# Optimization experiments

Hardware: AMD Instinct MI355X
Metric: run time of the kernel (lower is better)

Reference implementation:

```python
import jax, jax.numpy as jnp
import numpy as np

B, T, C, H = 4, 2048, 1024, 16
D = C // H  # head_dim = 64

def setup_inputs() -> dict:
    key = jax.random.key(0)
    k1, k2, k3 = jax.random.split(key, 3)
    x = jax.random.normal(k1, (B, T, C), dtype=jnp.float32)
    w_qkv = jax.random.normal(k2, (C, 3 * C), dtype=jnp.float32) * (C ** -0.5)
    w_proj = jax.random.normal(k3, (C, C), dtype=jnp.float32) * (C ** -0.5)
    b_proj = jnp.zeros((C,), dtype=jnp.float32)
    return {"x": x, "w_qkv": w_qkv, "w_proj": w_proj, "b_proj": b_proj}

def reference(x, w_qkv, w_proj, b_proj):
    Bx, Tx, Cx = x.shape
    qkv = x @ w_qkv  # [B,T,3C]
    q, k, v = jnp.split(qkv, 3, axis=-1)
    # [B,T,H,D] -> [B,H,T,D]
    q = q.reshape(Bx, Tx, H, D).transpose(0, 2, 1, 3)
    k = k.reshape(Bx, Tx, H, D).transpose(0, 2, 1, 3)
    v = v.reshape(Bx, Tx, H, D).transpose(0, 2, 1, 3)
    scale = 1.0 / np.sqrt(D).astype(np.float32)
    att = jnp.einsum('bhqd,bhkd->bhqk', q, k) * scale  # [B,H,T,T]
    causal = jnp.tril(jnp.ones((Tx, Tx), dtype=bool))
    att = jnp.where(causal, att, -jnp.inf)
    att = jax.nn.softmax(att, axis=-1)
    y = jnp.einsum('bhqk,bhkd->bhqd', att, v)  # [B,H,T,D]
    y = y.transpose(0, 2, 1, 3).reshape(Bx, Tx, Cx)
    return y @ w_proj + b_proj
```

## Files before the change

### kernel.cpp

```cpp
#include <hip/hip_runtime.h>

typedef unsigned short u16;
typedef unsigned int u32;
typedef __attribute__((ext_vector_type(2))) unsigned int u32x2;
typedef __attribute__((ext_vector_type(8))) short bf16x8;
typedef __attribute__((ext_vector_type(4))) float f32x4;
typedef __attribute__((ext_vector_type(16))) float f32x16;
typedef __attribute__((ext_vector_type(4))) unsigned short u16x4;

#define MFMA16(a, b, c) __builtin_amdgcn_mfma_f32_16x16x32_bf16((a), (b), (c), 0, 0, 0)
#define MFMA32(a, b, c) __builtin_amdgcn_mfma_f32_32x32x16_bf16((a), (b), (c), 0, 0, 0)

__device__ __forceinline__ u16 f2bf(float f) {
  union { float f; unsigned int i; } v; v.f = f;
  return (u16)((v.i + 0x7FFFu + ((v.i >> 16) & 1u)) >> 16);
}
__device__ __forceinline__ float exp2a(float x) {
  float r; asm("v_exp_f32 %0, %1" : "=v"(r) : "v"(x)); return r;
}
__device__ __forceinline__ u32 cvtpk(float lo, float hi) {
  u32 d; asm("v_cvt_pk_bf16_f32 %0, %1, %2" : "=v"(d) : "v"(lo), "v"(hi)); return d;
}
__device__ __forceinline__ void gl2lds16(const u16* g, u16* l) {
  __builtin_amdgcn_global_load_lds(
      (const __attribute__((address_space(1))) void*)g,
      (__attribute__((address_space(3))) void*)l, 16, 0, 0);
}

__global__ __launch_bounds__(256) void k_prep(const float* __restrict__ x,
                                              u16* __restrict__ xb,
                                              const float* __restrict__ w_qkv,
                                              u16* __restrict__ wqkvT,
                                              const float* __restrict__ w_proj,
                                              u16* __restrict__ wprojT) {
  const int id = (int)blockIdx.x;
  const int t = threadIdx.x;
  if (id < 4096) {
    const int i = id * 256 + t;
    const float* s = x + (size_t)i * 8;
    float4 a = *(const float4*)(s);
    float4 b = *(const float4*)(s + 4);
    union { u16 o[8]; int4 v; } u;
    u.o[0] = f2bf(a.x); u.o[1] = f2bf(a.y); u.o[2] = f2bf(a.z); u.o[3] = f2bf(a.w);
    u.o[4] = f2bf(b.x); u.o[5] = f2bf(b.y); u.o[6] = f2bf(b.z); u.o[7] = f2bf(b.w);
    *(int4*)(&xb[(size_t)i * 8]) = u.v;
    return;
  }
  __shared__ u16 tile[64][65];
  const float* src;
  u16* dst;
  int R, C, c0, r0;
  if (id < 4864) {
    const int q = id - 4096;
    src = w_qkv; dst = wqkvT; R = 1024; C = 3072;
    c0 = (q % 48) * 64; r0 = (q / 48) * 64;
  } else {
    const int q = id - 4864;
    src = w_proj; dst = wprojT; R = 1024; C = 1024;
    c0 = (q % 16) * 64; r0 = (q / 16) * 64;
  }
#pragma unroll
  for (int i = 0; i < 16; ++i) {
    int e = i * 256 + t, rr = e >> 6, cc = e & 63;
    tile[rr][cc] = f2bf(src[(size_t)(r0 + rr) * C + c0 + cc]);
  }
  __syncthreads();
#pragma unroll
  for (int i = 0; i < 16; ++i) {
    int e = i * 256 + t, rr = e >> 6, cc = e & 63;
    dst[(size_t)(c0 + rr) * R + r0 + cc] = tile[cc][rr];
  }
}

template <int QKV>
__global__ __launch_bounds__(256) void k_gemm(
    const u16* __restrict__ A, const u16* __restrict__ Bt,
    const float* __restrict__ bias, float* __restrict__ Cf,
    u16* __restrict__ Qb, u16* __restrict__ Kb, u16* __restrict__ VTb,
    int M, int N, int K, int BNn) {
  __shared__ __attribute__((aligned(16))) u16 As[128 * 32];
  __shared__ __attribute__((aligned(16))) u16 Bs[128 * 32];
  const int wg = (int)blockIdx.x;
  const int xcd = wg & 7, loc = wg >> 3;
  const int bmPerXcd = (M >> 7) >> 3;
  const int bm = xcd * bmPerXcd + loc / BNn;
  const int bn = loc % BNn;
  const int t = threadIdx.x, lane = t & 63, w = t >> 6;
  const int wr = w >> 1, wc = w & 1;
  const int rh = lane & 15, kg = lane >> 4;
  const int srow = lane >> 2, sk8 = (lane & 3) << 3;

  f32x4 acc[4][4];
#pragma unroll
  for (int mi = 0; mi < 4; ++mi)
#pragma unroll
    for (int ni = 0; ni < 4; ++ni) acc[mi][ni] = (f32x4)0.0f;

  for (int k0 = 0; k0 < K; k0 += 32) {
#pragma unroll
    for (int i = 0; i < 2; ++i) {
      const int r0 = w * 32 + i * 16;
      gl2lds16(&A[(size_t)(bm * 128 + r0 + srow) * K + k0 + sk8], &As[r0 * 32]);
      gl2lds16(&Bt[(size_t)(bn * 128 + r0 + srow) * K + k0 + sk8], &Bs[r0 * 32]);
    }
    asm volatile("s_waitcnt vmcnt(0)" ::: "memory");
    __syncthreads();

    bf16x8 af[4], bfr[4];
#pragma unroll
    for (int mi = 0; mi < 4; ++mi)
      af[mi] = *(const bf16x8*)(&As[(wr * 64 + mi * 16 + rh) * 32 + kg * 8]);
#pragma unroll
    for (int ni = 0; ni < 4; ++ni)
      bfr[ni] = *(const bf16x8*)(&Bs[(wc * 64 + ni * 16 + rh) * 32 + kg * 8]);
    __builtin_amdgcn_s_setprio(1);
#pragma unroll
    for (int mi = 0; mi < 4; ++mi)
#pragma unroll
      for (int ni = 0; ni < 4; ++ni)
        acc[mi][ni] = MFMA16(af[mi], bfr[ni], acc[mi][ni]);
    __builtin_amdgcn_s_setprio(0);
    __syncthreads();
  }

  if (QKV == 0) {
    const int rbase = bm * 128 + wr * 64;
    const int cbase = bn * 128 + wc * 64;
#pragma unroll
    for (int ni = 0; ni < 4; ++ni) {
      const int col = cbase + ni * 16 + rh;
      const float bv = bias ? bias[col] : 0.0f;
#pragma unroll
      for (int mi = 0; mi < 4; ++mi) {
#pragma unroll
        for (int r = 0; r < 4; ++r) {
          int row = rbase + mi * 16 + kg * 4 + r;
          Cf[(size_t)row * N + col] = acc[mi][ni][r] + bv;
        }
      }
    }
  } else {
    const float SCQ = 0.125f * 1.44269504f;
    const int rowbase = bm * 128 + wr * 64;
    const int b = rowbase >> 11;
    const int tb = rowbase & 2047;
    const int cbase = bn * 128 + wc * 64;
    const int role = cbase >> 10;
    const int h = (cbase & 1023) >> 6;
    const int bh = b * 16 + h;
#pragma unroll
    for (int ni = 0; ni < 4; ++ni) {
      const int d = ni * 16 + rh;
#pragma unroll
      for (int mi = 0; mi < 4; ++mi) {
        const int tt = tb + mi * 16 + kg * 4;
        if (role == 2) {
          u16x4 pk;
#pragma unroll
          for (int r = 0; r < 4; ++r) pk[r] = f2bf(acc[mi][ni][r]);
          *(u16x4*)(&VTb[((size_t)bh * 64 + d) * 2048 + tt]) = pk;
        } else {
          u16* dst = (role == 0) ? Qb : Kb;
          const float sc = (role == 0) ? SCQ : 1.0f;
#pragma unroll
          for (int r = 0; r < 4; ++r)
            dst[((size_t)bh * 2048 + tt + r) * 64 + d] = f2bf(acc[mi][ni][r] * sc);
        }
      }
    }
  }
}

__global__ __launch_bounds__(64, 2) void k_attn(const u16* __restrict__ Qb,
                                                const u16* __restrict__ Kb,
                                                const u16* __restrict__ VTb,
                                                u16* __restrict__ Y) {
  const int bh = blockIdx.x;
  const int sb = 31 - (int)blockIdx.y;
  const int lane = threadIdx.x & 63;
  const int q31 = lane & 31, hi = lane >> 5;
  const int qA = sb * 64 + q31;
  const int qBr = sb * 64 + 32 + q31;
  const u16* Qh = Qb + (size_t)bh * 2048 * 64;
  const u16* Kh = Kb + (size_t)bh * 2048 * 64;
  const u16* Vh = VTb + (size_t)bh * 64 * 2048;
  const int b = bh >> 4, h = bh & 15;

  bf16x8 qfA[4], qfB[4];
#pragma unroll
  for (int d = 0; d < 4; ++d) {
    qfA[d] = *(const bf16x8*)(&Qh[(size_t)qA * 64 + d * 16 + hi * 8]);
    qfB[d] = *(const bf16x8*)(&Qh[(size_t)qBr * 64 + d * 16 + hi * 8]);
  }

  f32x16 oA0 = (f32x16)0.0f, oA1 = (f32x16)0.0f;
  f32x16 oB0 = (f32x16)0.0f, oB1 = (f32x16)0.0f;
  float mA = -1e30f, sA = 0.0f, mB = -1e30f, sB = 0.0f;

  const int nt = 2 * sb + 2;
  bf16x8 kf[4];
#pragma unroll
  for (int d = 0; d < 4; ++d)
    kf[d] = *(const bf16x8*)(&Kh[(size_t)q31 * 64 + d * 16 + hi * 8]);

  for (int tt = 0; tt < nt; ++tt) {
    const int j0 = tt * 32;
    const bool aAct = tt < nt - 1;

    const int jn = (tt + 1 < nt) ? j0 + 32 : j0;
    bf16x8 kn[4];
#pragma unroll
    for (int d = 0; d < 4; ++d)
      kn[d] = *(const bf16x8*)(&Kh[(size_t)(jn + q31) * 64 + d * 16 + hi * 8]);
    const bf16x8 vf0 = *(const bf16x8*)(&Vh[(size_t)q31 * 2048 + j0 + hi * 8]);
    const bf16x8 vf1 = *(const bf16x8*)(&Vh[(size_t)q31 * 2048 + j0 + 16 + hi * 8]);
    const bf16x8 vf2 = *(const bf16x8*)(&Vh[(size_t)(32 + q31) * 2048 + j0 + hi * 8]);
    const bf16x8 vf3 = *(const bf16x8*)(&Vh[(size_t)(32 + q31) * 2048 + j0 + 16 + hi * 8]);

    f32x16 stB = (f32x16)0.0f;
    __builtin_amdgcn_s_setprio(1);
#pragma unroll
    for (int d = 0; d < 4; ++d) stB = MFMA32(kf[d], qfB[d], stB);
    f32x16 stA = (f32x16)0.0f;
    if (aAct) {
#pragma unroll
      for (int d = 0; d < 4; ++d) stA = MFMA32(kf[d], qfA[d], stA);
    }
    __builtin_amdgcn_s_setprio(0);

    if (tt == nt - 2) {
#pragma unroll
      for (int r = 0; r < 16; ++r) {
        const int kcol = (r & 3) + 8 * (r >> 2) + 4 * hi;
        if (kcol > q31) stA[r] = -1e30f;
      }
    }
    if (tt == nt - 1) {
#pragma unroll
      for (int r = 0; r < 16; ++r) {
        const int kcol = (r & 3) + 8 * (r >> 2) + 4 * hi;
        if (kcol > q31) stB[r] = -1e30f;
      }
    }

    union { u32 w4[4]; bf16x8 f; } paA0, paA1, paB0, paB1;
    if (aAct) {
      float mx = fmaxf(
          fmaxf(fmaxf(fmaxf(stA[0], stA[1]), fmaxf(stA[2], stA[3])),
                fmaxf(fmaxf(stA[4], stA[5]), fmaxf(stA[6], stA[7]))),
          fmaxf(fmaxf(fmaxf(stA[8], stA[9]), fmaxf(stA[10], stA[11])),
                fmaxf(fmaxf(stA[12], stA[13]), fmaxf(stA[14], stA[15]))));
      if (__any(mx - mA > 8.0f)) {
        mx = fmaxf(mx, __shfl_xor(mx, 32));
        const float mn = fmaxf(mA, mx);
        const float scf = exp2a(mA - mn);
        mA = mn; sA *= scf; oA0 *= scf; oA1 *= scf;
      }
      float p[16];
#pragma unroll
      for (int r = 0; r < 16; ++r) p[r] = exp2a(stA[r] - mA);
      sA += (((p[0] + p[1]) + (p[2] + p[3])) + ((p[4] + p[5]) + (p[6] + p[7]))) +
            (((p[8] + p[9]) + (p[10] + p[11])) + ((p[12] + p[13]) + (p[14] + p[15])));
      u32 D0 = cvtpk(p[0], p[1]),   D1 = cvtpk(p[2], p[3]);
      u32 D2 = cvtpk(p[4], p[5]),   D3 = cvtpk(p[6], p[7]);
      u32 D4 = cvtpk(p[8], p[9]),   D5 = cvtpk(p[10], p[11]);
      u32 D6 = cvtpk(p[12], p[13]), D7 = cvtpk(p[14], p[15]);
      u32x2 s02 = __builtin_amdgcn_permlane32_swap(D0, D2, false, false);
      u32x2 s13 = __builtin_amdgcn_permlane32_swap(D1, D3, false, false);
      u32x2 s46 = __builtin_amdgcn_permlane32_swap(D4, D6, false, false);
      u32x2 s57 = __builtin_amdgcn_permlane32_swap(D5, D7, false, false);
      paA0.w4[0] = s02.x; paA0.w4[1] = s13.x; paA0.w4[2] = s02.y; paA0.w4[3] = s13.y;
      paA1.w4[0] = s46.x; paA1.w4[1] = s57.x; paA1.w4[2] = s46.y; paA1.w4[3] = s57.y;
    }

    {
      float mx = fmaxf(
          fmaxf(fmaxf(fmaxf(stB[0], stB[1]), fmaxf(stB[2], stB[3])),
                fmaxf(fmaxf(stB[4], stB[5]), fmaxf(stB[6], stB[7]))),
          fmaxf(fmaxf(fmaxf(stB[8], stB[9]), fmaxf(stB[10], stB[11])),
                fmaxf(fmaxf(stB[12], stB[13]), fmaxf(stB[14], stB[15]))));
      if (__any(mx - mB > 8.0f)) {
        mx = fmaxf(mx, __shfl_xor(mx, 32));
        const float mn = fmaxf(mB, mx);
        const float scf = exp2a(mB - mn);
        mB = mn; sB *= scf; oB0 *= scf; oB1 *= scf;
      }
      float p[16];
#pragma unroll
      for (int r = 0; r < 16; ++r) p[r] = exp2a(stB[r] - mB);
      sB += (((p[0] + p[1]) + (p[2] + p[3])) + ((p[4] + p[5]) + (p[6] + p[7]))) +
            (((p[8] + p[9]) + (p[10] + p[11])) + ((p[12] + p[13]) + (p[14] + p[15])));
      u32 D0 = cvtpk(p[0], p[1]),   D1 = cvtpk(p[2], p[3]);
      u32 D2 = cvtpk(p[4], p[5]),   D3 = cvtpk(p[6], p[7]);
      u32 D4 = cvtpk(p[8], p[9]),   D5 = cvtpk(p[10], p[11]);
      u32 D6 = cvtpk(p[12], p[13]), D7 = cvtpk(p[14], p[15]);
      u32x2 s02 = __builtin_amdgcn_permlane32_swap(D0, D2, false, false);
      u32x2 s13 = __builtin_amdgcn_permlane32_swap(D1, D3, false, false);
      u32x2 s46 = __builtin_amdgcn_permlane32_swap(D4, D6, false, false);
      u32x2 s57 = __builtin_amdgcn_permlane32_swap(D5, D7, false, false);
      paB0.w4[0] = s02.x; paB0.w4[1] = s13.x; paB0.w4[2] = s02.y; paB0.w4[3] = s13.y;
      paB1.w4[0] = s46.x; paB1.w4[1] = s57.x; paB1.w4[2] = s46.y; paB1.w4[3] = s57.y;
    }

    __builtin_amdgcn_s_setprio(1);
    oB0 = MFMA32(vf0, paB0.f, oB0);
    oB0 = MFMA32(vf1, paB1.f, oB0);
    oB1 = MFMA32(vf2, paB0.f, oB1);
    oB1 = MFMA32(vf3, paB1.f, oB1);
    if (aAct) {
      oA0 = MFMA32(vf0, paA0.f, oA0);
      oA0 = MFMA32(vf1, paA1.f, oA0);
      oA1 = MFMA32(vf2, paA0.f, oA1);
      oA1 = MFMA32(vf3, paA1.f, oA1);
    }
    __builtin_amdgcn_s_setprio(0);

#pragma unroll
    for (int d = 0; d < 4; ++d) kf[d] = kn[d];
  }

  sA += __shfl_xor(sA, 32);
  sB += __shfl_xor(sB, 32);
  const float invA = 1.0f / sA, invB = 1.0f / sB;
  u16* yrowA = Y + ((size_t)b * 2048 + qA) * 1024 + h * 64;
  u16* yrowB = Y + ((size_t)b * 2048 + qBr) * 1024 + h * 64;
#pragma unroll
  for (int a = 0; a < 4; ++a) {
    u16x4 pk;
#pragma unroll
    for (int i = 0; i < 4; ++i) pk[i] = f2bf(oA0[a * 4 + i] * invA);
    *(u16x4*)(yrowA + a * 8 + 4 * hi) = pk;
#pragma unroll
    for (int i = 0; i < 4; ++i) pk[i] = f2bf(oA1[a * 4 + i] * invA);
    *(u16x4*)(yrowA + 32 + a * 8 + 4 * hi) = pk;
#pragma unroll
    for (int i = 0; i < 4; ++i) pk[i] = f2bf(oB0[a * 4 + i] * invB);
    *(u16x4*)(yrowB + a * 8 + 4 * hi) = pk;
#pragma unroll
    for (int i = 0; i < 4; ++i) pk[i] = f2bf(oB1[a * 4 + i] * invB);
    *(u16x4*)(yrowB + 32 + a * 8 + 4 * hi) = pk;
  }
}

extern "C" void kernel_launch(void* const* d_in, const int* in_sizes, int n_in,
                              void* d_out, int out_size, void* d_ws, size_t ws_size,
                              hipStream_t stream) {
  const float* x      = (const float*)d_in[0];
  const float* w_qkv  = (const float*)d_in[1];
  const float* w_proj = (const float*)d_in[2];
  const float* b_proj = (const float*)d_in[3];
  float* out = (float*)d_out;

  char* ws = (char*)d_ws;
  u16* wqkvT  = (u16*)(ws);
  u16* wprojT = (u16*)(ws + 6291456);
  u16* Qb     = (u16*)(ws + 8388608);
  u16* Kb     = (u16*)(ws + 25165824);
  u16* VTb    = (u16*)(ws + 41943040);
  u16* xb     = (u16*)(ws + 58720256);
  u16* Yb     = xb;

  k_prep<<<5120, 256, 0, stream>>>(x, xb, w_qkv, wqkvT, w_proj, wprojT);
  k_gemm<1><<<1536, 256, 0, stream>>>(xb, wqkvT, nullptr, nullptr,
                                      Qb, Kb, VTb, 8192, 3072, 1024, 24);
  k_attn<<<dim3(64, 32), 64, 0, stream>>>(Qb, Kb, VTb, Yb);
  k_gemm<0><<<512, 256, 0, stream>>>(Yb, wprojT, b_proj, out,
                                     nullptr, nullptr, nullptr, 8192, 1024, 1024, 8);
}
```

Measured before the change: 200.9 us.

## Software-pipeline attention loop so PV MFMAs of previous tile overlap current QK

Restructures the causal flash-attention inner loop into a prologue, steady state and epilogue. In the steady state the P·V MFMAs for the previous key tile are issued right after the Q·K MFMAs for the current tile. The softmax exp and convert work of one tile can then overlap matrix-core work of another, instead of serialising on the dependency chain. This costs extra live registers for the carried P fragments and duplicated code, which may raise VGPR pressure and reduce occupancy.

```diff
diff --git a/kernel.cpp b/kernel.cpp
--- a/kernel.cpp
+++ b/kernel.cpp
@@ -198,53 +198,36 @@
   float mA = -1e30f, sA = 0.0f, mB = -1e30f, sB = 0.0f;
 
   const int nt = 2 * sb + 2;
-  bf16x8 kf[4];
+  bf16x8 kf[4], kn[4];
 #pragma unroll
   for (int d = 0; d < 4; ++d)
     kf[d] = *(const bf16x8*)(&Kh[(size_t)q31 * 64 + d * 16 + hi * 8]);
 
-  for (int tt = 0; tt < nt; ++tt) {
-    const int j0 = tt * 32;
-    const bool aAct = tt < nt - 1;
-
-    const int jn = (tt + 1 < nt) ? j0 + 32 : j0;
-    bf16x8 kn[4];
+  union U { u32 w4[4]; bf16x8 f; };
+  U paA0, paA1, paB0, paB1;
+
+  {
 #pragma unroll
     for (int d = 0; d < 4; ++d)
-      kn[d] = *(const bf16x8*)(&Kh[(size_t)(jn + q31) * 64 + d * 16 + hi * 8]);
-    const bf16x8 vf0 = *(const bf16x8*)(&Vh[(size_t)q31 * 2048 + j0 + hi * 8]);
-    const bf16x8 vf1 = *(const bf16x8*)(&Vh[(size_t)q31 * 2048 + j0 + 16 + hi * 8]);
-    const bf16x8 vf2 = *(const bf16x8*)(&Vh[(size_t)(32 + q31) * 2048 + j0 + hi * 8]);
-    const bf16x8 vf3 = *(const bf16x8*)(&Vh[(size_t)(32 + q31) * 2048 + j0 + 16 + hi * 8]);
+      kn[d] = *(const bf16x8*)(&Kh[(size_t)(32 + q31) * 64 + d * 16 + hi * 8]);
 
     f32x16 stB = (f32x16)0.0f;
     __builtin_amdgcn_s_setprio(1);
 #pragma unroll
     for (int d = 0; d < 4; ++d) stB = MFMA32(kf[d], qfB[d], stB);
     f32x16 stA = (f32x16)0.0f;
-    if (aAct) {
-#pragma unroll
-      for (int d = 0; d < 4; ++d) stA = MFMA32(kf[d], qfA[d], stA);
-    }
+#pragma unroll
+    for (int d = 0; d < 4; ++d) stA = MFMA32(kf[d], qfA[d], stA);
     __builtin_amdgcn_s_setprio(0);
 
-    if (tt == nt - 2) {
+    if (nt == 2) {
 #pragma unroll
       for (int r = 0; r < 16; ++r) {
         const int kcol = (r & 3) + 8 * (r >> 2) + 4 * hi;
         if (kcol > q31) stA[r] = -1e30f;
       }
     }
-    if (tt == nt - 1) {
-#pragma unroll
-      for (int r = 0; r < 16; ++r) {
-        const int kcol = (r & 3) + 8 * (r >> 2) + 4 * hi;
-        if (kcol > q31) stB[r] = -1e30f;
-      }
-    }
-
-    union { u32 w4[4]; bf16x8 f; } paA0, paA1, paB0, paB1;
-    if (aAct) {
+    {
       float mx = fmaxf(
           fmaxf(fmaxf(fmaxf(stA[0], stA[1]), fmaxf(stA[2], stA[3])),
                 fmaxf(fmaxf(stA[4], stA[5]), fmaxf(stA[6], stA[7]))),
@@ -272,7 +255,6 @@
       paA0.w4[0] = s02.x; paA0.w4[1] = s13.x; paA0.w4[2] = s02.y; paA0.w4[3] = s13.y;
       paA1.w4[0] = s46.x; paA1.w4[1] = s57.x; paA1.w4[2] = s46.y; paA1.w4[3] = s57.y;
     }
-
     {
       float mx = fmaxf(
           fmaxf(fmaxf(fmaxf(stB[0], stB[1]), fmaxf(stB[2], stB[3])),
@@ -301,22 +283,131 @@
       paB0.w4[0] = s02.x; paB0.w4[1] = s13.x; paB0.w4[2] = s02.y; paB0.w4[3] = s13.y;
       paB1.w4[0] = s46.x; paB1.w4[1] = s57.x; paB1.w4[2] = s46.y; paB1.w4[3] = s57.y;
     }
-
+#pragma unroll
+    for (int d = 0; d < 4; ++d) kf[d] = kn[d];
+  }
+
+  for (int tt = 1; tt < nt; ++tt) {
+    const int jp = (tt - 1) * 32;
+    const int jn = (tt + 1 < nt) ? (tt + 1) * 32 : tt * 32;
+    const bool aAct = tt < nt - 1;
+
+    const bf16x8 vf0 = *(const bf16x8*)(&Vh[(size_t)q31 * 2048 + jp + hi * 8]);
+    const bf16x8 vf1 = *(const bf16x8*)(&Vh[(size_t)q31 * 2048 + jp + 16 + hi * 8]);
+    const bf16x8 vf2 = *(const bf16x8*)(&Vh[(size_t)(32 + q31) * 2048 + jp + hi * 8]);
+    const bf16x8 vf3 = *(const bf16x8*)(&Vh[(size_t)(32 + q31) * 2048 + jp + 16 + hi * 8]);
+#pragma unroll
+    for (int d = 0; d < 4; ++d)
+      kn[d] = *(const bf16x8*)(&Kh[(size_t)(jn + q31) * 64 + d * 16 + hi * 8]);
+
+    f32x16 stB = (f32x16)0.0f;
+    __builtin_amdgcn_s_setprio(1);
+#pragma unroll
+    for (int d = 0; d < 4; ++d) stB = MFMA32(kf[d], qfB[d], stB);
+    f32x16 stA = (f32x16)0.0f;
+    if (aAct) {
+#pragma unroll
+      for (int d = 0; d < 4; ++d) stA = MFMA32(kf[d], qfA[d], stA);
+    }
+    oB0 = MFMA32(vf0, paB0.f, oB0);
+    oB0 = MFMA32(vf1, paB1.f, oB0);
+    oB1 = MFMA32(vf2, paB0.f, oB1);
+    oB1 = MFMA32(vf3, paB1.f, oB1);
+    oA0 = MFMA32(vf0, paA0.f, oA0);
+    oA0 = MFMA32(vf1, paA1.f, oA0);
+    oA1 = MFMA32(vf2, paA0.f, oA1);
+    oA1 = MFMA32(vf3, paA1.f, oA1);
+    __builtin_amdgcn_s_setprio(0);
+
+    if (tt == nt - 2) {
+#pragma unroll
+      for (int r = 0; r < 16; ++r) {
+        const int kcol = (r & 3) + 8 * (r >> 2) + 4 * hi;
+        if (kcol > q31) stA[r] = -1e30f;
+      }
+    }
+    if (tt == nt - 1) {
+#pragma unroll
+      for (int r = 0; r < 16; ++r) {
+        const int kcol = (r & 3) + 8 * (r >> 2) + 4 * hi;
+        if (kcol > q31) stB[r] = -1e30f;
+      }
+    }
+
+    if (aAct) {
+      float mx = fmaxf(
+          fmaxf(fmaxf(fmaxf(stA[0], stA[1]), fmaxf(stA[2], stA[3])),
+                fmaxf(fmaxf(stA[4], stA[5]), fmaxf(stA[6], stA[7]))),
+          fmaxf(fmaxf(fmaxf(stA[8], stA[9]), fmaxf(stA[10], stA[11])),
+                fmaxf(fmaxf(stA[12], stA[13]), fmaxf(stA[14], stA[15]))));
+      if (__any(mx - mA > 8.0f)) {
+        mx = fmaxf(mx, __shfl_xor(mx, 32));
+        const float mn = fmaxf(mA, mx);
+        const float scf = exp2a(mA - mn);
+        mA = mn; sA *= scf; oA0 *= scf; oA1 *= scf;
+      }
+      float p[16];
+#pragma unroll
+      for (int r = 0; r < 16; ++r) p[r] = exp2a(stA[r] - mA);
+      sA += (((p[0] + p[1]) + (p[2] + p[3])) + ((p[4] + p[5]) + (p[6] + p[7]))) +
+            (((p[8] + p[9]) + (p[10] + p[11])) + ((p[12] + p[13]) + (p[14] + p[15])));
+      u32 D0 = cvtpk(p[0], p[1]),   D1 = cvtpk(p[2], p[3]);
+      u32 D2 = cvtpk(p[4], p[5]),   D3 = cvtpk(p[6], p[7]);
+      u32 D4 = cvtpk(p[8], p[9]),   D5 = cvtpk(p[10], p[11]);
+      u32 D6 = cvtpk(p[12], p[13]), D7 = cvtpk(p[14], p[15]);
+      u32x2 s02 = __builtin_amdgcn_permlane32_swap(D0, D2, false, false);
+      u32x2 s13 = __builtin_amdgcn_permlane32_swap(D1, D3, false, false);
+      u32x2 s46 = __builtin_amdgcn_permlane32_swap(D4, D6, false, false);
+      u32x2 s57 = __builtin_amdgcn_permlane32_swap(D5, D7, false, false);
+      paA0.w4[0] = s02.x; paA0.w4[1] = s13.x; paA0.w4[2] = s02.y; paA0.w4[3] = s13.y;
+      paA1.w4[0] = s46.x; paA1.w4[1] = s57.x; paA1.w4[2] = s46.y; paA1.w4[3] = s57.y;
+    }
+
+    {
+      float mx = fmaxf(
+          fmaxf(fmaxf(fmaxf(stB[0], stB[1]), fmaxf(stB[2], stB[3])),
+                fmaxf(fmaxf(stB[4], stB[5]), fmaxf(stB[6], stB[7]))),
+          fmaxf(fmaxf(fmaxf(stB[8], stB[9]), fmaxf(stB[10], stB[11])),
+                fmaxf(fmaxf(stB[12], stB[13]), fmaxf(stB[14], stB[15]))));
+      if (__any(mx - mB > 8.0f)) {
+        mx = fmaxf(mx, __shfl_xor(mx, 32));
+        const float mn = fmaxf(mB, mx);
+        const float scf = exp2a(mB - mn);
+        mB = mn; sB *= scf; oB0 *= scf; oB1 *= scf;
+      }
+      float p[16];
+#pragma unroll
+      for (int r = 0; r < 16; ++r) p[r] = exp2a(stB[r] - mB);
+      sB += (((p[0] + p[1]) + (p[2] + p[3])) + ((p[4] + p[5]) + (p[6] + p[7]))) +
+            (((p[8] + p[9]) + (p[10] + p[11])) + ((p[12] + p[13]) + (p[14] + p[15])));
+      u32 D0 = cvtpk(p[0], p[1]),   D1 = cvtpk(p[2], p[3]);
+      u32 D2 = cvtpk(p[4], p[5]),   D3 = cvtpk(p[6], p[7]);
+      u32 D4 = cvtpk(p[8], p[9]),   D5 = cvtpk(p[10], p[11]);
+      u32 D6 = cvtpk(p[12], p[13]), D7 = cvtpk(p[14], p[15]);
+      u32x2 s02 = __builtin_amdgcn_permlane32_swap(D0, D2, false, false);
+      u32x2 s13 = __builtin_amdgcn_permlane32_swap(D1, D3, false, false);
+      u32x2 s46 = __builtin_amdgcn_permlane32_swap(D4, D6, false, false);
+      u32x2 s57 = __builtin_amdgcn_permlane32_swap(D5, D7, false, false);
+      paB0.w4[0] = s02.x; paB0.w4[1] = s13.x; paB0.w4[2] = s02.y; paB0.w4[3] = s13.y;
+      paB1.w4[0] = s46.x; paB1.w4[1] = s57.x; paB1.w4[2] = s46.y; paB1.w4[3] = s57.y;
+    }
+
+#pragma unroll
+    for (int d = 0; d < 4; ++d) kf[d] = kn[d];
+  }
+
+  {
+    const int jp = (nt - 1) * 32;
+    const bf16x8 vf0 = *(const bf16x8*)(&Vh[(size_t)q31 * 2048 + jp + hi * 8]);
+    const bf16x8 vf1 = *(const bf16x8*)(&Vh[(size_t)q31 * 2048 + jp + 16 + hi * 8]);
+    const bf16x8 vf2 = *(const bf16x8*)(&Vh[(size_t)(32 + q31) * 2048 + jp + hi * 8]);
+    const bf16x8 vf3 = *(const bf16x8*)(&Vh[(size_t)(32 + q31) * 2048 + jp + 16 + hi * 8]);
     __builtin_amdgcn_s_setprio(1);
     oB0 = MFMA32(vf0, paB0.f, oB0);
     oB0 = MFMA32(vf1, paB1.f, oB0);
     oB1 = MFMA32(vf2, paB0.f, oB1);
     oB1 = MFMA32(vf3, paB1.f, oB1);
-    if (aAct) {
-      oA0 = MFMA32(vf0, paA0.f, oA0);
-      oA0 = MFMA32(vf1, paA1.f, oA0);
-      oA1 = MFMA32(vf2, paA0.f, oA1);
-      oA1 = MFMA32(vf3, paA1.f, oA1);
-    }
     __builtin_amdgcn_s_setprio(0);
-
-#pragma unroll
-    for (int d = 0; d < 4; ++d) kf[d] = kn[d];
   }
 
   sA += __shfl_xor(sA, 32);
```

Result: no change. 202.9 us (+1.0%).
